# Performance work log

Measured on AMD Instinct MI355X. Metric: run time of the kernel, lower is better.

## Reference

```python
import jax, jax.numpy as jnp
import numpy as np

EMBED_DIM = 1024
NUM_HEADS = 16
HEAD_DIM = EMBED_DIM // NUM_HEADS


def setup_inputs() -> dict:
    key = jax.random.key(0)
    k1, k2, k3, k4 = jax.random.split(key, 4)
    scale = 1.0 / np.sqrt(EMBED_DIM)
    x = jax.random.normal(k1, (2, 2048, EMBED_DIM), dtype=jnp.float32)
    Wqkv = jax.random.normal(k2, (3 * EMBED_DIM, EMBED_DIM), dtype=jnp.float32) * scale
    Wproj = jax.random.normal(k3, (EMBED_DIM, EMBED_DIM), dtype=jnp.float32) * scale
    bproj = jax.random.normal(k4, (EMBED_DIM,), dtype=jnp.float32) * 0.01
    return {"x": x, "Wqkv": Wqkv, "Wproj": Wproj, "bproj": bproj}


def reference(x, Wqkv, Wproj, bproj):
    B, T, D = x.shape
    # QKV projection (torch Linear: x @ W.T), no bias
    qkv = jnp.einsum('btd,ed->bte', x, Wqkv)              # [B, T, 3D]
    qkv = qkv.reshape(B, T, 3, NUM_HEADS, HEAD_DIM)
    qkv = jnp.transpose(qkv, (2, 0, 3, 1, 4))             # [3, B, H, T, hd]
    q, k, v = qkv[0], qkv[1], qkv[2]
    # scaled dot-product attention (full matrix, as in source)
    dots = jnp.einsum('bhqd,bhkd->bhqk', q, k) / jnp.sqrt(jnp.asarray(HEAD_DIM, x.dtype))
    attn = jax.nn.softmax(dots, axis=-1)
    out = jnp.einsum('bhqk,bhkd->bhqd', attn, v)          # [B, H, T, hd]
    out = jnp.transpose(out, (0, 2, 1, 3)).reshape(B, T, D)
    # output projection with bias
    return jnp.einsum('btd,ed->bte', out, Wproj) + bproj
```

## Files before the change

kernel.cpp:

```cpp
#include <hip/hip_runtime.h>

typedef __attribute__((ext_vector_type(8))) short bf16x8;
typedef __attribute__((ext_vector_type(4))) short bf16x4;
typedef __attribute__((ext_vector_type(4))) float f32x4;
typedef __attribute__((ext_vector_type(2))) unsigned int u32x2;

#define MFMA32(a, b, c) __builtin_amdgcn_mfma_f32_16x16x32_bf16((a), (b), (c), 0, 0, 0)
#define MFMA16K(a, b, c) __builtin_amdgcn_mfma_f32_16x16x16bf16_1k((a), (b), (c), 0, 0, 0)

__device__ __forceinline__ unsigned short f2bf(float f) {
    unsigned u = __builtin_bit_cast(unsigned, f);
    u = (u + 0x7fffu + ((u >> 16) & 1u)) >> 16;
    return (unsigned short)u;
}

__device__ __forceinline__ unsigned cvtpk(float lo, float hi) {
    unsigned r;
    asm("v_cvt_pk_bf16_f32 %0, %1, %2" : "=v"(r) : "v"(lo), "v"(hi));
    return r;
}

__device__ __forceinline__ void gll16(const void* g, void* l) {
    __builtin_amdgcn_global_load_lds((__attribute__((address_space(1))) void*)g,
                                     (__attribute__((address_space(3))) void*)l,
                                     16, 0, 0);
}

__global__ __launch_bounds__(256) void castall(const float* __restrict__ x,
                                               const float* __restrict__ wqkv,
                                               const float* __restrict__ wproj,
                                               unsigned short* __restrict__ xb,
                                               unsigned short* __restrict__ wqkvb,
                                               unsigned short* __restrict__ wprojb) {
    const int N0 = 1048576, N1 = 786432, N2 = 262144;
    int stride = gridDim.x * blockDim.x;
    for (int i = blockIdx.x * blockDim.x + threadIdx.x; i < N0 + N1 + N2; i += stride) {
        const float4* s;
        ushort4* d;
        int k;
        if (i < N0) { s = (const float4*)x; d = (ushort4*)xb; k = i; }
        else if (i < N0 + N1) { s = (const float4*)wqkv; d = (ushort4*)wqkvb; k = i - N0; }
        else { s = (const float4*)wproj; d = (ushort4*)wprojb; k = i - N0 - N1; }
        float4 v = s[k];
        ushort4 o;
        o.x = f2bf(v.x); o.y = f2bf(v.y); o.z = f2bf(v.z); o.w = f2bf(v.w);
        d[k] = o;
    }
}

template <int EPI, int TN>
__global__ __launch_bounds__(256) void gemm_bt(const unsigned short* __restrict__ A,
                                               const unsigned short* __restrict__ B,
                                               int K,
                                               unsigned short* __restrict__ qbuf,
                                               unsigned short* __restrict__ kbuf,
                                               unsigned short* __restrict__ vtb,
                                               float* __restrict__ outF,
                                               const float* __restrict__ bias) {
    __shared__ __align__(16) unsigned short As[2][4096];
    __shared__ __align__(16) unsigned short Bs[2][TN * 32];
    const int tid = threadIdx.x;
    const int w = tid >> 6, l = tid & 63;
    const int g = l >> 4, cc = l & 15;
    constexpr int MI = (TN == 128) ? 4 : 2;
    const int wr = (TN == 128) ? (w >> 1) : w;
    const int wc = (TN == 128) ? (w & 1) : 0;

    const int nwg = gridDim.x * gridDim.y;
    const int lin = blockIdx.y * gridDim.x + blockIdx.x;
    const int swz = (lin & 7) * (nwg >> 3) + (lin >> 3);
    const int bx = swz % gridDim.x, by = swz / gridDim.x;
    const int m0 = by * 128, n0 = bx * TN;

    f32x4 acc[MI][4];
#pragma unroll
    for (int i = 0; i < MI; ++i)
#pragma unroll
        for (int j = 0; j < 4; ++j) acc[i][j] = (f32x4){0.f, 0.f, 0.f, 0.f};

    const int srow = (l >> 2);
    const int skk = ((l & 3) ^ ((l >> 3) & 3)) * 8;
    const int gsw = (g ^ ((cc >> 1) & 3)) * 8;

#define GSTAGE(bb, k0)                                                              \
    do {                                                                            \
        _Pragma("unroll") for (int ch = 0; ch < 2; ++ch) {                          \
            int ci = ch * 4 + w;                                                    \
            gll16(A + (size_t)(m0 + ci * 16 + srow) * K + (k0) + skk,               \
                  &As[bb][ci * 512]);                                               \
        }                                                                           \
        if constexpr (TN == 128) {                                                  \
            _Pragma("unroll") for (int ch = 0; ch < 2; ++ch) {                      \
                int ci = ch * 4 + w;                                                \
                gll16(B + (size_t)(n0 + ci * 16 + srow) * K + (k0) + skk,           \
                      &Bs[bb][ci * 512]);                                           \
            }                                                                       \
        } else {                                                                    \
            gll16(B + (size_t)(n0 + w * 16 + srow) * K + (k0) + skk,                \
                  &Bs[bb][w * 512]);                                                \
        }                                                                           \
    } while (0)

    GSTAGE(0, 0);
    asm volatile("s_waitcnt vmcnt(0)" ::: "memory");
    __syncthreads();

    const int nt = K >> 5;
    int cur = 0;
    for (int t = 0; t < nt; ++t) {
        if (t + 1 < nt) GSTAGE(cur ^ 1, (t + 1) * 32);
        bf16x8 af[MI], bfr[4];
#pragma unroll
        for (int i = 0; i < MI; ++i)
            af[i] = *(const bf16x8*)&As[cur][(wr * (MI * 16) + i * 16 + cc) * 32 + gsw];
#pragma unroll
        for (int j = 0; j < 4; ++j)
            bfr[j] = *(const bf16x8*)&Bs[cur][(wc * 64 + j * 16 + cc) * 32 + gsw];
        __builtin_amdgcn_s_setprio(1);
#pragma unroll
        for (int i = 0; i < MI; ++i)
#pragma unroll
            for (int j = 0; j < 4; ++j) acc[i][j] = MFMA32(af[i], bfr[j], acc[i][j]);
        __builtin_amdgcn_s_setprio(0);
        asm volatile("s_waitcnt vmcnt(0)" ::: "memory");
        __syncthreads();
        cur ^= 1;
    }
#undef GSTAGE

    if (EPI == 0) {
        const int which = n0 >> 10;
#pragma unroll
        for (int jn = 0; jn < 4; ++jn) {
            int n = n0 + wc * 64 + jn * 16 + cc;
            int hn = n & 1023;
            int h = hn >> 6, d = hn & 63;
#pragma unroll
            for (int i = 0; i < MI; ++i) {
#pragma unroll
                for (int j = 0; j < 4; ++j) {
                    int m = m0 + wr * (MI * 16) + i * 16 + g * 4 + j;
                    int b = m >> 11, t = m & 2047;
                    int bh = b * 16 + h;
                    float v = acc[i][jn][j];
                    if (which == 0) {
                        qbuf[((size_t)bh * 2048 + t) * 64 + d] = f2bf(v * 0.1803368801f);
                    } else if (which == 1) {
                        kbuf[((size_t)bh * 2048 + t) * 64 + d] = f2bf(v);
                    } else {
                        vtb[((size_t)bh * 64 + d) * 2048 + t] = f2bf(v);
                    }
                }
            }
        }
    } else {
#pragma unroll
        for (int jn = 0; jn < 4; ++jn) {
            int n = n0 + wc * 64 + jn * 16 + cc;
            float bn = bias[n];
#pragma unroll
            for (int i = 0; i < MI; ++i) {
#pragma unroll
                for (int j = 0; j < 4; ++j) {
                    int m = m0 + wr * (MI * 16) + i * 16 + g * 4 + j;
                    outF[(size_t)m * 1024 + n] = acc[i][jn][j] + bn;
                }
            }
        }
    }
}

__global__ __launch_bounds__(512, 4) void attn_kernel(const unsigned short* __restrict__ qb,
                                                      const unsigned short* __restrict__ kb,
                                                      const unsigned short* __restrict__ vtb,
                                                      unsigned short* __restrict__ ao) {
    __shared__ __align__(16) unsigned short smem[32768];
    const int bh = blockIdx.y;
    const int w = threadIdx.x >> 6, l = threadIdx.x & 63;
    const int g = l >> 4, cc = l & 15;
    const int grp = w >> 2, wq = w & 3;
    const int q0 = blockIdx.x * 128 + wq * 32;
    const int kvoff = grp * 1024;

    const unsigned short* qbase = qb + (size_t)bh * 2048 * 64;
    const unsigned short* kbase = kb + (size_t)bh * 2048 * 64;
    const unsigned short* vbase = vtb + (size_t)bh * 64 * 2048;

    const int sl8 = l >> 3, sl7 = l & 7;
    const int sperm = ((sl7 ^ sl8) * 8);

#define STAGE(bb, kk)                                                                          \
    do {                                                                                       \
        int base = grp * 16384 + (bb) * 8192;                                                  \
        gll16(kbase + (size_t)((kk) + wq * 8 + sl8) * 64 + sperm, &smem[base + wq * 512]);     \
        gll16(kbase + (size_t)((kk) + (wq + 4) * 8 + sl8) * 64 + sperm,                        \
              &smem[base + (wq + 4) * 512]);                                                   \
        gll16(vbase + (size_t)(wq * 8 + sl8) * 2048 + (kk) + sperm,                            \
              &smem[base + 4096 + wq * 512]);                                                  \
        gll16(vbase + (size_t)((wq + 4) * 8 + sl8) * 2048 + (kk) + sperm,                      \
              &smem[base + 4096 + (wq + 4) * 512]);                                            \
    } while (0)

    bf16x8 qf[2][2];
#pragma unroll
    for (int qt = 0; qt < 2; ++qt)
#pragma unroll
        for (int kh = 0; kh < 2; ++kh)
            qf[qt][kh] = *(const bf16x8*)(qbase + (size_t)(q0 + qt * 16 + cc) * 64 + kh * 32 + g * 8);

    float lrun[2] = {0.f, 0.f};
    f32x4 acc[2][4];
#pragma unroll
    for (int qt = 0; qt < 2; ++qt)
#pragma unroll
        for (int dt = 0; dt < 4; ++dt) acc[qt][dt] = (f32x4){0.f, 0.f, 0.f, 0.f};

    const int swz = cc & 7;

    STAGE(0, kvoff);
    asm volatile("s_waitcnt vmcnt(0)" ::: "memory");
    __syncthreads();

    for (int t = 0; t < 16; ++t) {
        const int cb = t & 1;
        if (t + 1 < 16) STAGE(cb ^ 1, kvoff + (t + 1) * 64);

        const unsigned short* Kb = &smem[grp * 16384 + cb * 8192];
        const unsigned short* Vb = Kb + 4096;

        bf16x8 kf[4][2];
#pragma unroll
        for (int kt = 0; kt < 4; ++kt)
#pragma unroll
            for (int kh = 0; kh < 2; ++kh)
                kf[kt][kh] = *(const bf16x8*)&Kb[(kt * 16 + cc) * 64 + (((kh * 4 + g) ^ swz) * 8)];

        f32x4 s[2][4];
        __builtin_amdgcn_s_setprio(1);
#pragma unroll
        for (int qt = 0; qt < 2; ++qt)
#pragma unroll
            for (int kt = 0; kt < 4; ++kt) {
                f32x4 z = (f32x4){0.f, 0.f, 0.f, 0.f};
                z = MFMA32(kf[kt][0], qf[qt][0], z);
                z = MFMA32(kf[kt][1], qf[qt][1], z);
                s[qt][kt] = z;
            }
        __builtin_amdgcn_s_setprio(0);

        bf16x4 pf[2][4];
#pragma unroll
        for (int qt = 0; qt < 2; ++qt) {
#pragma unroll
            for (int kt = 0; kt < 4; ++kt) {
                float p0 = __builtin_amdgcn_exp2f(s[qt][kt][0]);
                float p1 = __builtin_amdgcn_exp2f(s[qt][kt][1]);
                float p2 = __builtin_amdgcn_exp2f(s[qt][kt][2]);
                float p3 = __builtin_amdgcn_exp2f(s[qt][kt][3]);
                lrun[qt] += (p0 + p1) + (p2 + p3);
                u32x2 wv;
                wv.x = cvtpk(p0, p1);
                wv.y = cvtpk(p2, p3);
                pf[qt][kt] = __builtin_bit_cast(bf16x4, wv);
            }
        }

        __builtin_amdgcn_s_setprio(1);
#pragma unroll
        for (int kt = 0; kt < 4; ++kt) {
            const int seg = ((kt * 2 + (g >> 1)) ^ swz);
#pragma unroll
            for (int dt = 0; dt < 4; ++dt) {
                bf16x4 vf = *(const bf16x4*)&Vb[(dt * 16 + cc) * 64 + seg * 8 + (g & 1) * 4];
                acc[0][dt] = MFMA16K(vf, pf[0][kt], acc[0][dt]);
                acc[1][dt] = MFMA16K(vf, pf[1][kt], acc[1][dt]);
            }
        }
        __builtin_amdgcn_s_setprio(0);

        asm volatile("s_waitcnt vmcnt(0)" ::: "memory");
        __syncthreads();
    }
#undef STAGE

    float lsum[2];
#pragma unroll
    for (int qt = 0; qt < 2; ++qt) {
        float v = lrun[qt];
        v += __shfl_xor(v, 16);
        v += __shfl_xor(v, 32);
        lsum[qt] = v;
    }

    float* cs = (float*)smem;
    const int slot = (wq * 64 + l) * 35;
    if (grp == 1) {
#pragma unroll
        for (int qt = 0; qt < 2; ++qt)
#pragma unroll
            for (int dt = 0; dt < 4; ++dt)
#pragma unroll
                for (int j = 0; j < 4; ++j) cs[slot + (qt * 4 + dt) * 4 + j] = acc[qt][dt][j];
        cs[slot + 32] = lsum[0];
        cs[slot + 33] = lsum[1];
    }
    __syncthreads();
    if (grp == 0) {
        const int b = bh >> 4, h = bh & 15;
#pragma unroll
        for (int qt = 0; qt < 2; ++qt) {
            float inv = 1.f / (lsum[qt] + cs[slot + 32 + qt]);
            size_t rowbase = ((size_t)(b * 2048 + q0 + qt * 16 + cc)) * 1024 + h * 64;
#pragma unroll
            for (int dt = 0; dt < 4; ++dt) {
                float r0 = acc[qt][dt][0] + cs[slot + (qt * 4 + dt) * 4 + 0];
                float r1 = acc[qt][dt][1] + cs[slot + (qt * 4 + dt) * 4 + 1];
                float r2 = acc[qt][dt][2] + cs[slot + (qt * 4 + dt) * 4 + 2];
                float r3 = acc[qt][dt][3] + cs[slot + (qt * 4 + dt) * 4 + 3];
                u32x2 ov;
                ov.x = cvtpk(r0 * inv, r1 * inv);
                ov.y = cvtpk(r2 * inv, r3 * inv);
                *(u32x2*)(ao + rowbase + dt * 16 + g * 4) = ov;
            }
        }
    }
}

extern "C" void kernel_launch(void* const* d_in, const int* in_sizes, int n_in,
                              void* d_out, int out_size, void* d_ws, size_t ws_size,
                              hipStream_t stream) {
    const float* x = (const float*)d_in[0];
    const float* Wqkv = (const float*)d_in[1];
    const float* Wproj = (const float*)d_in[2];
    const float* bproj = (const float*)d_in[3];
    float* out = (float*)d_out;

    unsigned short* xb = (unsigned short*)d_ws;
    unsigned short* wqkvb = xb + 4096 * 1024;
    unsigned short* wprojb = wqkvb + 3072 * 1024;
    unsigned short* qbuf = wprojb + 1024 * 1024;
    unsigned short* kbuf = qbuf + 32 * 2048 * 64;
    unsigned short* vtb = kbuf + 32 * 2048 * 64;
    unsigned short* aob = vtb + 32 * 2048 * 64;

    castall<<<2048, 256, 0, stream>>>(x, Wqkv, Wproj, xb, wqkvb, wprojb);

    gemm_bt<0, 128><<<dim3(24, 32), 256, 0, stream>>>(xb, wqkvb, 1024, qbuf, kbuf, vtb, nullptr, nullptr);
    attn_kernel<<<dim3(16, 32), 512, 0, stream>>>(qbuf, kbuf, vtb, aob);
    gemm_bt<1, 64><<<dim3(16, 32), 256, 0, stream>>>(aob, wprojb, 1024, nullptr, nullptr, nullptr, out, bproj);
}
```

Before: 186.4 us.

## Triple-buffer GEMM LDS staging and vectorize V-transpose epilogue stores

The projection GEMM moves from a double-buffered to a triple-buffered LDS pipeline. Loads are issued two tiles ahead, and each step waits on a partial vmcnt before a raw s_barrier, instead of draining all loads every iteration. Separately, the V-transpose epilogue packs four consecutive-token accumulators into two bf16 pairs with cvt_pk and writes them as one 8-byte store. This replaces four scattered 2-byte stores. LDS use grows by half, which may lower occupancy, and the partial-wait counts have to match the number of loads each stage issues.

```diff
diff --git a/kernel.cpp b/kernel.cpp
--- a/kernel.cpp
+++ b/kernel.cpp
@@ -57,8 +57,8 @@
                                                unsigned short* __restrict__ vtb,
                                                float* __restrict__ outF,
                                                const float* __restrict__ bias) {
-    __shared__ __align__(16) unsigned short As[2][4096];
-    __shared__ __align__(16) unsigned short Bs[2][TN * 32];
+    __shared__ __align__(16) unsigned short As[3][4096];
+    __shared__ __align__(16) unsigned short Bs[3][TN * 32];
     const int tid = threadIdx.x;
     const int w = tid >> 6, l = tid & 63;
     const int g = l >> 4, cc = l & 15;
@@ -101,14 +101,22 @@
         }                                                                           \
     } while (0)
 
+#define WAITLD()                                                                    \
+    do {                                                                            \
+        if constexpr (TN == 128) asm volatile("s_waitcnt vmcnt(4)" ::: "memory");   \
+        else                     asm volatile("s_waitcnt vmcnt(3)" ::: "memory");   \
+    } while (0)
+
+    const int nt = K >> 5;
     GSTAGE(0, 0);
-    asm volatile("s_waitcnt vmcnt(0)" ::: "memory");
-    __syncthreads();
-
-    const int nt = K >> 5;
-    int cur = 0;
+    GSTAGE(1, 32);
+    WAITLD();
+    __builtin_amdgcn_s_barrier();
+    __builtin_amdgcn_sched_barrier(0);
+
+    int cur = 0, stg = 2;
     for (int t = 0; t < nt; ++t) {
-        if (t + 1 < nt) GSTAGE(cur ^ 1, (t + 1) * 32);
+        if (t + 2 < nt) GSTAGE(stg, (t + 2) * 32);
         bf16x8 af[MI], bfr[4];
 #pragma unroll
         for (int i = 0; i < MI; ++i)
@@ -122,33 +130,56 @@
 #pragma unroll
             for (int j = 0; j < 4; ++j) acc[i][j] = MFMA32(af[i], bfr[j], acc[i][j]);
         __builtin_amdgcn_s_setprio(0);
-        asm volatile("s_waitcnt vmcnt(0)" ::: "memory");
-        __syncthreads();
-        cur ^= 1;
+        if (t + 1 < nt) {
+            if (t + 2 < nt) WAITLD();
+            else asm volatile("s_waitcnt vmcnt(0)" ::: "memory");
+            __builtin_amdgcn_s_barrier();
+            __builtin_amdgcn_sched_barrier(0);
+        }
+        cur = (cur == 2) ? 0 : cur + 1;
+        stg = (stg == 2) ? 0 : stg + 1;
     }
 #undef GSTAGE
+#undef WAITLD
 
     if (EPI == 0) {
         const int which = n0 >> 10;
-#pragma unroll
-        for (int jn = 0; jn < 4; ++jn) {
-            int n = n0 + wc * 64 + jn * 16 + cc;
-            int hn = n & 1023;
-            int h = hn >> 6, d = hn & 63;
-#pragma unroll
-            for (int i = 0; i < MI; ++i) {
-#pragma unroll
-                for (int j = 0; j < 4; ++j) {
-                    int m = m0 + wr * (MI * 16) + i * 16 + g * 4 + j;
+        if (which == 2) {
+#pragma unroll
+            for (int jn = 0; jn < 4; ++jn) {
+                int n = n0 + wc * 64 + jn * 16 + cc;
+                int hn = n & 1023;
+                int h = hn >> 6, d = hn & 63;
+#pragma unroll
+                for (int i = 0; i < MI; ++i) {
+                    int m = m0 + wr * (MI * 16) + i * 16 + g * 4;
                     int b = m >> 11, t = m & 2047;
                     int bh = b * 16 + h;
-                    float v = acc[i][jn][j];
-                    if (which == 0) {
-                        qbuf[((size_t)bh * 2048 + t) * 64 + d] = f2bf(v * 0.1803368801f);
-                    } else if (which == 1) {
-                        kbuf[((size_t)bh * 2048 + t) * 64 + d] = f2bf(v);
-                    } else {
-                        vtb[((size_t)bh * 64 + d) * 2048 + t] = f2bf(v);
+                    u32x2 pv;
+                    pv.x = cvtpk(acc[i][jn][0], acc[i][jn][1]);
+                    pv.y = cvtpk(acc[i][jn][2], acc[i][jn][3]);
+                    *(u32x2*)(vtb + ((size_t)bh * 64 + d) * 2048 + t) = pv;
+                }
+            }
+        } else {
+#pragma unroll
+            for (int jn = 0; jn < 4; ++jn) {
+                int n = n0 + wc * 64 + jn * 16 + cc;
+                int hn = n & 1023;
+                int h = hn >> 6, d = hn & 63;
+#pragma unroll
+                for (int i = 0; i < MI; ++i) {
+#pragma unroll
+                    for (int j = 0; j < 4; ++j) {
+                        int m = m0 + wr * (MI * 16) + i * 16 + g * 4 + j;
+                        int b = m >> 11, t = m & 2047;
+                        int bh = b * 16 + h;
+                        float v = acc[i][jn][j];
+                        if (which == 0) {
+                            qbuf[((size_t)bh * 2048 + t) * 64 + d] = f2bf(v * 0.1803368801f);
+                        } else {
+                            kbuf[((size_t)bh * 2048 + t) * 64 + d] = f2bf(v);
+                        }
                     }
                 }
             }
```

Result: no change. 188.8 us (+1.3%).
